# Kernel tuning notes

Measured on AMD Instinct MI355X. Metric: run time of the kernel, lower is better.

The kernel has to match this reference:

```python
import jax, jax.numpy as jnp
import numpy as np
from fractions import Fraction
from math import factorial

MUL = 64
IRREPS = [(MUL, 0, 1), (MUL, 1, -1), (MUL, 2, 1)]  # (mul, l, parity); same for in1/in2/out
N = 4096


def _f(n):
    return Fraction(factorial(round(n)), 1)


def _su2_cg(j1, m1, j2, m2, j3, m3):
    # Complex-basis SU(2) Clebsch-Gordan coefficient <j1 m1 j2 m2 | j3 m3> (Racah formula).
    if m3 != m1 + m2:
        return 0.0
    vmin = int(max(-j1 + j2 + m3, -j1 + m1, 0))
    vmax = int(min(j2 + j3 + m1, j3 - j1 + j2, j3 + m3))
    C = float((2 * j3 + 1) * Fraction(
        _f(j3 + j1 - j2) * _f(j3 - j1 + j2) * _f(j1 + j2 - j3) * _f(j3 + m3) * _f(j3 - m3),
        _f(j1 + j2 + j3 + 1) * _f(j1 - m1) * _f(j1 + m1) * _f(j2 - m2) * _f(j2 + m2))) ** 0.5
    S = Fraction(0)
    for v in range(vmin, vmax + 1):
        S += (-1) ** int(v + j2 + m2) * Fraction(
            _f(j2 + j3 + m1 - v) * _f(j1 - m1 + v),
            _f(v) * _f(j3 - j1 + j2 - v) * _f(j3 + m3 - v) * _f(v + j1 - j2 - m3))
    return C * float(S)


def _q(l):
    # Change of basis real -> complex spherical harmonics, with (-i)^l phase so CG is real.
    q = np.zeros((2 * l + 1, 2 * l + 1), dtype=complex)
    for m in range(-l, 0):
        q[l + m, l + abs(m)] = 1 / 2 ** 0.5
        q[l + m, l - abs(m)] = -1j / 2 ** 0.5
    q[l, l] = 1
    for m in range(1, l + 1):
        q[l + m, l + abs(m)] = (-1) ** m / 2 ** 0.5
        q[l + m, l - abs(m)] = 1j * (-1) ** m / 2 ** 0.5
    return (-1j) ** l * q


def _so3_cg(l1, l2, l3):
    # Real-basis SO(3) Clebsch-Gordan tensor, shape (2l1+1, 2l2+1, 2l3+1).
    C = np.zeros((2 * l1 + 1, 2 * l2 + 1, 2 * l3 + 1))
    for m1 in range(-l1, l1 + 1):
        for m2 in range(-l2, l2 + 1):
            for m3 in range(-l3, l3 + 1):
                C[l1 + m1, l2 + m2, l3 + m3] = _su2_cg(l1, m1, l2, m2, l3, m3)
    C = np.einsum('ij,kl,mn,ikm->jln', _q(l1), _q(l2), np.conj(_q(l3)), C)
    assert np.abs(C.imag).max() < 1e-6
    return np.ascontiguousarray(C.real.astype(np.float32))


def _offsets(irreps):
    offs, o = [], 0
    for mul, l, p in irreps:
        offs.append(o)
        o += mul * (2 * l + 1)
    return offs, o


OFF, DIM = _offsets(IRREPS)

# Enumerate fully-connected paths honoring parity and triangle selection rules.
PATHS = []
for io, (mo, lo, po) in enumerate(IRREPS):
    for i1, (m1, l1, p1) in enumerate(IRREPS):
        for i2, (m2, l2, p2) in enumerate(IRREPS):
            if p1 * p2 == po and abs(l1 - l2) <= lo <= l1 + l2:
                PATHS.append((i1, i2, io, _so3_cg(l1, l2, lo)))
N_PATHS = len(PATHS)  # 11 for this irrep layout


def setup_inputs() -> dict:
    key = jax.random.key(0)
    k1, k2, k3 = jax.random.split(key, 3)
    inputs1 = jax.random.normal(k1, (N, DIM), dtype=jnp.float32)
    inputs2 = jax.random.normal(k2, (N, DIM), dtype=jnp.float32)
    std = 1.0 / float(np.sqrt(MUL * MUL))  # per-path weight_std
    W = jax.random.normal(k3, (N_PATHS, MUL, MUL, MUL), dtype=jnp.float32) * std
    return {"inputs1": inputs1, "inputs2": inputs2, "W": W}


def _seg(x, i):
    mul, l, _ = IRREPS[i]
    d = 2 * l + 1
    return x[:, OFF[i]:OFF[i] + mul * d].reshape(x.shape[0], mul, d)


def reference(inputs1, inputs2, W):
    # out[z, w, k] = sum_{u,v,i,j} W_path[u,v,w] * CG[i,j,k] * x1[z,u,i] * x2[z,v,j]
    segs = [[] for _ in IRREPS]
    for p, (i1, i2, io, cg) in enumerate(PATHS):
        x1 = _seg(inputs1, i1)  # [z, u, i]
        x2 = _seg(inputs2, i2)  # [z, v, j]
        y = jnp.einsum('zui,zvj,ijk,uvw->zwk', x1, x2, jnp.asarray(cg), W[p], optimize=True)
        segs[io].append(y)
    out = jnp.concatenate(
        [sum(s).reshape(inputs1.shape[0], -1) for s in segs], axis=-1)
    # normalize=True: divide by sqrt(output dim), as in the source
    return out * (1.0 / float(np.sqrt(out.shape[-1])))
```

## Files before the change

kernel.cpp:

```cpp
#include <hip/hip_runtime.h>
#include <hip/hip_fp16.h>


typedef unsigned short u16;
typedef _Float16 f16;
typedef __attribute__((ext_vector_type(8))) _Float16 f16x8;
typedef __attribute__((ext_vector_type(4))) float f32x4;

#define NZ 4096
#define ROWE 832
#define ROW2 576

__device__ __forceinline__ u16 f2h(float x) {
    _Float16 v = (_Float16)x; u16 b; __builtin_memcpy(&b, &v, 2); return b;
}

constexpr u16 f2h_bits(float xf) {
    unsigned u = __builtin_bit_cast(unsigned, xf);
    unsigned sign = (u >> 16) & 0x8000u;
    int exp = (int)((u >> 23) & 0xffu) - 127 + 15;
    unsigned man = u & 0x7fffffu;
    if (exp >= 31) return (u16)(sign | 0x7c00u);
    if (exp <= 0) {
        if (exp < -10) return (u16)sign;
        man |= 0x800000u;
        int sh = 14 - exp;
        unsigned h = man >> sh;
        unsigned rem = man & ((1u << sh) - 1u);
        unsigned half = 1u << (sh - 1);
        if (rem > half || (rem == half && (h & 1u))) ++h;
        return (u16)(sign | h);
    }
    unsigned h = ((unsigned)exp << 10) | (man >> 13);
    unsigned rem = man & 0x1fffu;
    if (rem > 0x1000u || (rem == 0x1000u && (h & 1u))) ++h;
    return (u16)(sign | h);
}
__device__ __forceinline__ __half2 h2dup(unsigned bits16) {
    unsigned d = bits16 * 0x10001u;
    __half2 r; __builtin_memcpy(&r, &d, 4); return r;
}
__device__ __forceinline__ __half2 h2zero() {
    unsigned z = 0; __half2 r; __builtin_memcpy(&r, &z, 4); return r;
}

struct CGE { int i, j, k; float c; };
template<int P> struct CGT;
template<> struct CGT<0> { static constexpr int n=1; static constexpr CGE e[1]={{0,0,0,1.0f}}; };
template<> struct CGT<1> { static constexpr int n=3; static constexpr CGE e[3]={
    {0,0,0,0.5773502691896258f},{1,1,0,0.5773502691896258f},{2,2,0,0.5773502691896258f}}; };
template<> struct CGT<2> { static constexpr int n=5; static constexpr CGE e[5]={
    {0,0,0,0.4472135954999579f},{1,1,0,0.4472135954999579f},{2,2,0,0.4472135954999579f},
    {3,3,0,0.4472135954999579f},{4,4,0,0.4472135954999579f}}; };
template<> struct CGT<3> { static constexpr int n=3; static constexpr CGE e[3]={
    {0,0,0,1.0f},{0,1,1,1.0f},{0,2,2,1.0f}}; };
template<> struct CGT<4> { static constexpr int n=3; static constexpr CGE e[3]={
    {0,0,0,1.0f},{1,0,1,1.0f},{2,0,2,1.0f}}; };
template<> struct CGT<5> { static constexpr int n=11; static constexpr CGE e[11]={
    {0,2,0,-0.31622776601683794f},{1,1,0,0.5477225575051661f},{0,4,0,-0.5477225575051661f},{2,0,0,0.5477225575051661f},
    {0,1,1,0.5477225575051661f},{2,3,1,0.5477225575051661f},{1,2,1,0.6324555320336759f},
    {2,2,2,-0.31622776601683794f},{1,3,2,0.5477225575051661f},{0,0,2,0.5477225575051661f},{2,4,2,0.5477225575051661f}}; };
template<> struct CGT<6> { static constexpr int n=11; static constexpr CGE e[11]={
    {2,0,0,-0.31622776601683794f},{1,1,0,0.5477225575051661f},{4,0,0,-0.5477225575051661f},{0,2,0,0.5477225575051661f},
    {1,0,1,0.5477225575051661f},{3,2,1,0.5477225575051661f},{2,1,1,0.6324555320336759f},
    {2,2,2,-0.31622776601683794f},{3,1,2,0.5477225575051661f},{0,0,2,0.5477225575051661f},{4,2,2,0.5477225575051661f}}; };
template<> struct CGT<7> { static constexpr int n=5; static constexpr CGE e[5]={
    {0,0,0,1.0f},{0,1,1,1.0f},{0,2,2,1.0f},{0,3,3,1.0f},{0,4,4,1.0f}}; };
template<> struct CGT<8> { static constexpr int n=11; static constexpr CGE e[11]={
    {0,2,0,0.7071067811865476f},{2,0,0,0.7071067811865476f},
    {0,1,1,0.7071067811865476f},{1,0,1,0.7071067811865476f},
    {0,0,2,-0.4082482904638630f},{1,1,2,0.8164965809277260f},{2,2,2,-0.4082482904638630f},
    {1,2,3,0.7071067811865476f},{2,1,3,0.7071067811865476f},
    {0,0,4,-0.7071067811865476f},{2,2,4,0.7071067811865476f}}; };
template<> struct CGT<9> { static constexpr int n=5; static constexpr CGE e[5]={
    {0,0,0,1.0f},{1,0,1,1.0f},{2,0,2,1.0f},{3,0,3,1.0f},{4,0,4,1.0f}}; };
template<> struct CGT<10> { static constexpr int n=25; static constexpr CGE e[25]={
    {0,2,0,-0.5345224838248488f},{2,0,0,-0.5345224838248488f},{1,3,0,0.4629100498862757f},{3,1,0,0.4629100498862757f},
    {0,3,1,0.4629100498862757f},{3,0,1,0.4629100498862757f},{1,4,1,-0.4629100498862757f},{4,1,1,-0.4629100498862757f},
    {1,2,1,0.2672612419124244f},{2,1,1,0.2672612419124244f},
    {0,0,2,-0.5345224838248488f},{1,1,2,0.2672612419124244f},{2,2,2,0.5345224838248488f},{3,3,2,0.2672612419124244f},{4,4,2,-0.5345224838248488f},
    {0,1,3,0.4629100498862757f},{1,0,3,0.4629100498862757f},{3,4,3,0.4629100498862757f},{4,3,3,0.4629100498862757f},
    {2,3,3,0.2672612419124244f},{3,2,3,0.2672612419124244f},
    {1,1,4,-0.4629100498862757f},{3,3,4,0.4629100498862757f},{2,4,4,-0.5345224838248488f},{4,2,4,-0.5345224838248488f}}; };

template<int SEG>
__device__ __forceinline__ int soff(int m) {
    if constexpr (SEG == 0) return m;
    else if constexpr (SEG == 1) return 64 + 4*m;
    else return 320 + 8*m;
}
template<int SEG>
__device__ __forceinline__ int sb2(int j) {
    if constexpr (SEG == 0) return 0;
    else if constexpr (SEG == 1) return 64 + j*64;
    else return 256 + j*64;
}
template<int L>
__device__ __forceinline__ void load_a1bits(const u16* p, u16* o) {
    if constexpr (L == 0) {
        o[0] = p[0];
    } else if constexpr (L == 1) {
        uint2 r = *reinterpret_cast<const uint2*>(p);
        o[0] = (u16)(r.x & 0xffff); o[1] = (u16)(r.x >> 16); o[2] = (u16)(r.y & 0xffff);
    } else {
        uint4 r = *reinterpret_cast<const uint4*>(p);
        o[0] = (u16)(r.x & 0xffff); o[1] = (u16)(r.x >> 16);
        o[2] = (u16)(r.y & 0xffff); o[3] = (u16)(r.y >> 16);
        o[4] = (u16)(r.z & 0xffff);
    }
}

__device__ __forceinline__ void stage_chunk(const u16* __restrict__ Wtb, int g,
                                            u16* lbuf, int tid) {
    const u16* src = Wtb + ((size_t)g << 13);
    #pragma unroll
    for (int qq = 0; qq < 4; ++qq) {
        const int off = qq*2048 + tid*8;
        __builtin_amdgcn_global_load_lds(
            (const __attribute__((address_space(1))) void*)(const void*)(src + off),
            (__attribute__((address_space(3))) void*)(void*)(lbuf + off),
            16, 0, 0);
    }
}

template<int PID, int S1, int S2, int KO>
__device__ __forceinline__ void chunk_compute(const u16* __restrict__ lbuf,
                                              const u16 (&a1b)[2][2*S1+1],
                                              const __half2 (&b2h)[2][4][2*S2+1],
                                              f32x4 (&acc)[KO][4], int lane) {
    const int kb = lane >> 4, nl = lane & 15;
    #pragma unroll
    for (int uu = 0; uu < 2; ++uu) {
        __half2 a1h[2*S1+1];
        #pragma unroll
        for (int i = 0; i < 2*S1+1; ++i) a1h[i] = h2dup(a1b[uu][i]);
        __half2 pre[CGT<PID>::n];
        #pragma unroll
        for (int t = 0; t < CGT<PID>::n; ++t) {
            const u16 cb = f2h_bits(CGT<PID>::e[t].c);
            pre[t] = __hmul2(h2dup(cb), a1h[CGT<PID>::e[t].i]);
        }
        #pragma unroll
        for (int h = 0; h < 2; ++h) {
            f16x8 bf[4];
            #pragma unroll
            for (int nf = 0; nf < 4; ++nf) {
                const int w = nf*16 + nl;
                const int slot = w*16 + ((uu*8 + h*4 + kb) ^ (w & 15));
                bf[nf] = *reinterpret_cast<const f16x8*>(lbuf + slot*8);
            }
            #pragma unroll
            for (int ko = 0; ko < KO; ++ko) {
                union { __half2 h[4]; f16x8 v; } af;
                #pragma unroll
                for (int q = 0; q < 4; ++q) {
                    __half2 s = h2zero();
                    #pragma unroll
                    for (int t = 0; t < CGT<PID>::n; ++t)
                        if (CGT<PID>::e[t].k == ko)
                            s = __hfma2(pre[t], b2h[h][q][CGT<PID>::e[t].j], s);
                    af.h[q] = s;
                }
                #pragma unroll
                for (int nf = 0; nf < 4; ++nf)
                    acc[ko][nf] = __builtin_amdgcn_mfma_f32_16x16x32_f16(af.v, bf[nf], acc[ko][nf], 0, 0, 0);
            }
        }
    }
}

template<int PID, int S1, int S2, int KO>
__device__ __forceinline__ void run_path(const u16* __restrict__ x1r, const u16* __restrict__ x2r,
                                         const u16* __restrict__ Wtb, u16* lds,
                                         f32x4 (&acc)[KO][4], int lane, int tid,
                                         int cbase, int cpp, int& q, int nq, int GB) {
    constexpr int D1 = 2*S1 + 1, D2 = 2*S2 + 1;
    const int kb = lane >> 4;
    __half2 b2h[2][4][D2];
    #pragma unroll
    for (int h = 0; h < 2; ++h)
        #pragma unroll
        for (int j = 0; j < D2; ++j) {
            const u16* p = x2r + sb2<S2>(j) + h*32 + kb*8;
            uint4 r = *reinterpret_cast<const uint4*>(p);
            __builtin_memcpy(&b2h[h][0][j], &r.x, 4);
            __builtin_memcpy(&b2h[h][1][j], &r.y, 4);
            __builtin_memcpy(&b2h[h][2][j], &r.z, 4);
            __builtin_memcpy(&b2h[h][3][j], &r.w, 4);
        }

    const int ubase = cbase*2;
    u16 a1b[2][D1], a1nb[2][D1];
    #pragma unroll
    for (int uu = 0; uu < 2; ++uu)
        load_a1bits<S1>(x1r + soff<S1>(ubase + uu), a1b[uu]);

    for (int c = 0; c < cpp; ++c) {
        __syncthreads();
        const int cn = (c + 1 == cpp) ? 0 : c + 1;
        #pragma unroll
        for (int uu = 0; uu < 2; ++uu)
            load_a1bits<S1>(x1r + soff<S1>(ubase + cn*2 + uu), a1nb[uu]);
        if (q + 1 < nq) {
            const int qn = q + 1;
            const int g = GB + (qn/cpp)*32 + cbase + (qn % cpp);
            stage_chunk(Wtb, g, lds + ((qn & 1) << 13), tid);
        }
        chunk_compute<PID,S1,S2,KO>(lds + ((q & 1) << 13), a1b, b2h, acc, lane);
        #pragma unroll
        for (int uu = 0; uu < 2; ++uu)
            #pragma unroll
            for (int d = 0; d < D1; ++d) a1b[uu][d] = a1nb[uu][d];
        ++q;
    }
}

template<int IO, bool DIRECT>
__device__ __forceinline__ void run_unit(const u16* __restrict__ XB1, const u16* __restrict__ XB2,
                                         const u16* __restrict__ Wtb, float* __restrict__ dst,
                                         int zt, int cbase, int cpp, u16* lds) {
    constexpr int KO   = 2*IO + 1;
    constexpr int NP   = (IO == 0) ? 3 : 4;
    constexpr int GB   = (IO == 0) ? 0 : (IO == 1 ? 96 : 224);
    constexpr int OFFI = (IO == 0) ? 0 : (IO == 1 ? 64 : 256);
    constexpr int CO   = KO*64;
    const int tid = threadIdx.x;
    const int lane = tid & 63, wave = tid >> 6;
    const int zin = zt*64 + wave*16 + (lane & 15);
    const u16* x1r = XB1 + (size_t)zin*ROWE;
    const u16* x2r = XB2 + (size_t)zin*ROW2;
    f32x4 acc[KO][4];
    #pragma unroll
    for (int k = 0; k < KO; ++k)
        #pragma unroll
        for (int nf = 0; nf < 4; ++nf) acc[k][nf] = (f32x4){0.f, 0.f, 0.f, 0.f};

    int q = 0;
    const int nq = NP*cpp;
    stage_chunk(Wtb, GB + cbase, lds, tid);

    if constexpr (IO == 0) {
        run_path<0,0,0,KO>(x1r, x2r, Wtb, lds, acc, lane, tid, cbase, cpp, q, nq, GB);
        run_path<1,1,1,KO>(x1r, x2r, Wtb, lds, acc, lane, tid, cbase, cpp, q, nq, GB);
        run_path<2,2,2,KO>(x1r, x2r, Wtb, lds, acc, lane, tid, cbase, cpp, q, nq, GB);
    } else if constexpr (IO == 1) {
        run_path<3,0,1,KO>(x1r, x2r, Wtb, lds, acc, lane, tid, cbase, cpp, q, nq, GB);
        run_path<4,1,0,KO>(x1r, x2r, Wtb, lds, acc, lane, tid, cbase, cpp, q, nq, GB);
        run_path<5,1,2,KO>(x1r, x2r, Wtb, lds, acc, lane, tid, cbase, cpp, q, nq, GB);
        run_path<6,2,1,KO>(x1r, x2r, Wtb, lds, acc, lane, tid, cbase, cpp, q, nq, GB);
    } else {
        run_path<7,0,2,KO>(x1r, x2r, Wtb, lds, acc, lane, tid, cbase, cpp, q, nq, GB);
        run_path<8,1,1,KO>(x1r, x2r, Wtb, lds, acc, lane, tid, cbase, cpp, q, nq, GB);
        run_path<9,2,0,KO>(x1r, x2r, Wtb, lds, acc, lane, tid, cbase, cpp, q, nq, GB);
        run_path<10,2,2,KO>(x1r, x2r, Wtb, lds, acc, lane, tid, cbase, cpp, q, nq, GB);
    }

    float* lf = reinterpret_cast<float*>(lds);
    const int nl = lane & 15;
    const int hi = lane >> 4;
    #pragma unroll
    for (int round = 0; round < 4; ++round) {
        __syncthreads();
        if (wave == round) {
            const int zl = hi*4;
            #pragma unroll
            for (int k = 0; k < KO; ++k)
                #pragma unroll
                for (int nf = 0; nf < 4; ++nf) {
                    const int col = (nf*16 + nl)*KO + k;
                    #pragma unroll
                    for (int r = 0; r < 4; ++r)
                        lf[(zl + r)*CO + col] = acc[k][nf][r];
                }
        }
        __syncthreads();
        const int zbase = zt*64 + round*16;
        const int TOT4 = 4*CO;
        for (int i = tid; i < TOT4; i += 256) {
            const int zr = i / (CO/4), c4 = i % (CO/4);
            float4 v = *reinterpret_cast<const float4*>(&lf[zr*CO + c4*4]);
            if constexpr (DIRECT) {
                const float sc = 0.041666666666666664f;
                v.x *= sc; v.y *= sc; v.z *= sc; v.w *= sc;
            }
            *reinterpret_cast<float4*>(&dst[(size_t)(zbase + zr)*576 + OFFI + c4*4]) = v;
        }
    }
}

template<bool DIRECT>
__global__ __launch_bounds__(256) void tp_main(const u16* __restrict__ XB1, const u16* __restrict__ XB2,
                                               const u16* __restrict__ Wtb, float* __restrict__ dst) {
    __shared__ u16 smem[2*8192];
    const int bid = blockIdx.x;
    int io, uq, zt, cbase, cpp;
    if constexpr (DIRECT) {
        io = 2 - (bid >> 6); zt = bid & 63; uq = 0; cbase = 0; cpp = 32;
    } else {
        if (bid < 256)      { io = 2; uq = bid >> 6;         zt = bid & 63; cbase = uq*8; cpp = 8; }
        else if (bid < 448) { int b = bid - 256; io = 1; uq = b >> 6; zt = b & 63;
                              cbase = (uq == 0) ? 0 : (11 + 11*(uq - 1)); cpp = (uq == 2) ? 10 : 11; }
        else                { int b = bid - 448; io = 0; uq = 0; zt = b; cbase = 0; cpp = 32; }
    }
    float* dstP = DIRECT ? dst : dst + (size_t)uq*NZ*576;
    if (io == 0)      run_unit<0,DIRECT>(XB1, XB2, Wtb, dstP, zt, cbase, cpp, smem);
    else if (io == 1) run_unit<1,DIRECT>(XB1, XB2, Wtb, dstP, zt, cbase, cpp, smem);
    else              run_unit<2,DIRECT>(XB1, XB2, Wtb, dstP, zt, cbase, cpp, smem);
}

__global__ __launch_bounds__(256) void reduce_k(const float* __restrict__ P, float* __restrict__ out) {
    const int i = blockIdx.x*256 + threadIdx.x;
    const int col0 = (i*4) % 576;
    const int cnt = (col0 < 64) ? 1 : (col0 < 256 ? 3 : 4);
    float4 s = reinterpret_cast<const float4*>(P)[i];
    for (int u = 1; u < cnt; ++u) {
        float4 t = reinterpret_cast<const float4*>(P + (size_t)u*NZ*576)[i];
        s.x += t.x; s.y += t.y; s.z += t.z; s.w += t.w;
    }
    const float sc = 0.041666666666666664f;
    float4 o; o.x = s.x*sc; o.y = s.y*sc; o.z = s.z*sc; o.w = s.w*sc;
    reinterpret_cast<float4*>(out)[i] = o;
}

__global__ void prep_x(const float* __restrict__ x1, const float* __restrict__ x2,
                       u16* __restrict__ XB1, u16* __restrict__ XB2) {
    int g = blockIdx.x * 256 + threadIdx.x;
    const int P1 = NZ * 192;
    const int P2 = NZ * 144;
    if (g < P1) {
        const int zz = g / 192, s = g - zz*192, seg = s >> 6, m = s & 63;
        const float* sp = x1 + (size_t)zz*576;
        u16* dp = XB1 + (size_t)zz*ROWE;
        if (seg == 0) {
            dp[m] = f2h(sp[m]);
        } else if (seg == 1) {
            u16 t0 = f2h(sp[64 + m*3 + 0]);
            u16 t1 = f2h(sp[64 + m*3 + 1]);
            u16 t2 = f2h(sp[64 + m*3 + 2]);
            uint2 pk; pk.x = (unsigned)t0 | ((unsigned)t1 << 16); pk.y = (unsigned)t2;
            *reinterpret_cast<uint2*>(dp + 64 + m*4) = pk;
        } else {
            u16 t[5];
            #pragma unroll
            for (int c = 0; c < 5; ++c) t[c] = f2h(sp[256 + m*5 + c]);
            uint4 pk;
            pk.x = (unsigned)t[0] | ((unsigned)t[1] << 16);
            pk.y = (unsigned)t[2] | ((unsigned)t[3] << 16);
            pk.z = (unsigned)t[4];
            pk.w = 0u;
            *reinterpret_cast<uint4*>(dp + 320 + m*8) = pk;
        }
    } else if (g < P1 + P2) {
        const int gg = g - P1;
        const int zz = gg / 144, c4 = gg - zz*144;
        const int col = c4*4;
        const float* sp = x2 + (size_t)zz*576;
        u16 t[4];
        #pragma unroll
        for (int qd = 0; qd < 4; ++qd) {
            const int cc = col + qd;
            int si;
            if (cc < 64)       si = cc;
            else if (cc < 256) { const int j = (cc - 64) >> 6, v = (cc - 64) & 63;  si = 64  + v*3 + j; }
            else               { const int j = (cc - 256) >> 6, v = (cc - 256) & 63; si = 256 + v*5 + j; }
            t[qd] = f2h(sp[si]);
        }
        uint2 pk;
        pk.x = (unsigned)t[0] | ((unsigned)t[1] << 16);
        pk.y = (unsigned)t[2] | ((unsigned)t[3] << 16);
        *reinterpret_cast<uint2*>(XB2 + (size_t)zz*ROW2 + col) = pk;
    }
}

__global__ void prep_w(const float* __restrict__ W, u16* __restrict__ Wtb) {
    __shared__ float ld[4096];
    const int b = blockIdx.x;
    const int p = b >> 6, u = b & 63;
    const int tid = threadIdx.x;
    const float* src = W + ((size_t)(p*64 + u) << 12);
    #pragma unroll
    for (int i = 0; i < 16; ++i) ld[tid + i*256] = src[tid + i*256];
    __syncthreads();
    const int g  = p*32 + (u >> 1);
    const int mb = (u & 1)*8;
    #pragma unroll
    for (int r = 0; r < 2; ++r) {
        const int j = r*256 + tid;
        const int w = j & 63, ms = j >> 6;
        const int m = mb + ms;
        const int h = ms >> 2, kb = ms & 3;
        const int vb = h*32 + kb*8;
        u16 tmp[8];
        #pragma unroll
        for (int e = 0; e < 8; ++e) tmp[e] = f2h(ld[(vb + e)*64 + w]);
        const int unit = w*16 + (m ^ (w & 15));
        uint4 pk;
        pk.x = (unsigned)tmp[0] | ((unsigned)tmp[1] << 16);
        pk.y = (unsigned)tmp[2] | ((unsigned)tmp[3] << 16);
        pk.z = (unsigned)tmp[4] | ((unsigned)tmp[5] << 16);
        pk.w = (unsigned)tmp[6] | ((unsigned)tmp[7] << 16);
        *reinterpret_cast<uint4*>(Wtb + (size_t)g*8192 + (size_t)unit*8) = pk;
    }
}

extern "C" void kernel_launch(void* const* d_in, const int* in_sizes, int n_in,
                              void* d_out, int out_size, void* d_ws, size_t ws_size,
                              hipStream_t stream) {
    const float* x1 = (const float*)d_in[0];
    const float* x2 = (const float*)d_in[1];
    const float* W  = (const float*)d_in[2];
    float* out = (float*)d_out;

    u16* XB1 = (u16*)d_ws;
    u16* XB2 = XB1 + (size_t)NZ*ROWE;
    u16* Wtb = XB2 + (size_t)NZ*ROW2;
    const size_t baseu = (size_t)NZ*ROWE + (size_t)NZ*ROW2 + (size_t)11*32*8192;
    if (ws_size < baseu*2) return;
    float* Pbuf = (float*)(XB1 + baseu);
    const size_t avail = ws_size - baseu*2;
    const size_t psz = (size_t)NZ*576*4;
    const bool balanced = (avail >= 4*psz);

    hipLaunchKernelGGL(prep_x, dim3((NZ*(192+144))/256), dim3(256), 0, stream, x1, x2, XB1, XB2);
    hipLaunchKernelGGL(prep_w, dim3(11*64), dim3(256), 0, stream, W, Wtb);

    if (balanced) {
        hipLaunchKernelGGL(tp_main<false>, dim3(512), dim3(256), 0, stream, XB1, XB2, Wtb, Pbuf);
        hipLaunchKernelGGL(reduce_k, dim3(NZ*576/4/256), dim3(256), 0, stream, Pbuf, out);
    } else {
        hipLaunchKernelGGL(tp_main<true>, dim3(192), dim3(256), 0, stream, XB1, XB2, Wtb, out);
    }
}
```

Measured before the change: 112.7 us.

## Split output m-components across blocks and write split-K partials directly

The main kernel's work is repartitioned so each block handles only a subrange of output m-components (KOB..KOE). This doubles the grid from 512 to 1024 blocks and shrinks the accumulator register footprint per block. The l=0 output is now split into two u-halves, so reduce_k sums two partials for those columns. Non-bounce units store accumulators straight to global memory instead of staging through LDS. This removes syncs but gives strided scalar stores, and each split block repeats the x-operand and CG preprocessing.

```diff
diff --git a/kernel.cpp b/kernel.cpp
--- a/kernel.cpp
+++ b/kernel.cpp
@@ -123,11 +123,11 @@
     }
 }
 
-template<int PID, int S1, int S2, int KO>
+template<int PID, int S1, int S2, int KOB, int KOE>
 __device__ __forceinline__ void chunk_compute(const u16* __restrict__ lbuf,
                                               const u16 (&a1b)[2][2*S1+1],
                                               const __half2 (&b2h)[2][4][2*S2+1],
-                                              f32x4 (&acc)[KO][4], int lane) {
+                                              f32x4 (&acc)[KOE-KOB][4], int lane) {
     const int kb = lane >> 4, nl = lane & 15;
     #pragma unroll
     for (int uu = 0; uu < 2; ++uu) {
@@ -150,29 +150,29 @@
                 bf[nf] = *reinterpret_cast<const f16x8*>(lbuf + slot*8);
             }
             #pragma unroll
-            for (int ko = 0; ko < KO; ++ko) {
+            for (int koi = 0; koi < KOE-KOB; ++koi) {
                 union { __half2 h[4]; f16x8 v; } af;
                 #pragma unroll
                 for (int q = 0; q < 4; ++q) {
                     __half2 s = h2zero();
                     #pragma unroll
                     for (int t = 0; t < CGT<PID>::n; ++t)
-                        if (CGT<PID>::e[t].k == ko)
+                        if (CGT<PID>::e[t].k == KOB + koi)
                             s = __hfma2(pre[t], b2h[h][q][CGT<PID>::e[t].j], s);
                     af.h[q] = s;
                 }
                 #pragma unroll
                 for (int nf = 0; nf < 4; ++nf)
-                    acc[ko][nf] = __builtin_amdgcn_mfma_f32_16x16x32_f16(af.v, bf[nf], acc[ko][nf], 0, 0, 0);
+                    acc[koi][nf] = __builtin_amdgcn_mfma_f32_16x16x32_f16(af.v, bf[nf], acc[koi][nf], 0, 0, 0);
             }
         }
     }
 }
 
-template<int PID, int S1, int S2, int KO>
+template<int PID, int S1, int S2, int KOB, int KOE>
 __device__ __forceinline__ void run_path(const u16* __restrict__ x1r, const u16* __restrict__ x2r,
                                          const u16* __restrict__ Wtb, u16* lds,
-                                         f32x4 (&acc)[KO][4], int lane, int tid,
+                                         f32x4 (&acc)[KOE-KOB][4], int lane, int tid,
                                          int cbase, int cpp, int& q, int nq, int GB) {
     constexpr int D1 = 2*S1 + 1, D2 = 2*S2 + 1;
     const int kb = lane >> 4;
@@ -206,7 +206,7 @@
             const int g = GB + (qn/cpp)*32 + cbase + (qn % cpp);
             stage_chunk(Wtb, g, lds + ((qn & 1) << 13), tid);
         }
-        chunk_compute<PID,S1,S2,KO>(lds + ((q & 1) << 13), a1b, b2h, acc, lane);
+        chunk_compute<PID,S1,S2,KOB,KOE>(lds + ((q & 1) << 13), a1b, b2h, acc, lane);
         #pragma unroll
         for (int uu = 0; uu < 2; ++uu)
             #pragma unroll
@@ -215,7 +215,7 @@
     }
 }
 
-template<int IO, bool DIRECT>
+template<int IO, int KOB, int KOE, bool BOUNCE, bool DIRECT>
 __device__ __forceinline__ void run_unit(const u16* __restrict__ XB1, const u16* __restrict__ XB2,
                                          const u16* __restrict__ Wtb, float* __restrict__ dst,
                                          int zt, int cbase, int cpp, u16* lds) {
@@ -223,15 +223,15 @@
     constexpr int NP   = (IO == 0) ? 3 : 4;
     constexpr int GB   = (IO == 0) ? 0 : (IO == 1 ? 96 : 224);
     constexpr int OFFI = (IO == 0) ? 0 : (IO == 1 ? 64 : 256);
-    constexpr int CO   = KO*64;
+    constexpr int NK   = KOE - KOB;
     const int tid = threadIdx.x;
     const int lane = tid & 63, wave = tid >> 6;
     const int zin = zt*64 + wave*16 + (lane & 15);
     const u16* x1r = XB1 + (size_t)zin*ROWE;
     const u16* x2r = XB2 + (size_t)zin*ROW2;
-    f32x4 acc[KO][4];
-    #pragma unroll
-    for (int k = 0; k < KO; ++k)
+    f32x4 acc[NK][4];
+    #pragma unroll
+    for (int k = 0; k < NK; ++k)
         #pragma unroll
         for (int nf = 0; nf < 4; ++nf) acc[k][nf] = (f32x4){0.f, 0.f, 0.f, 0.f};
 
@@ -240,78 +240,104 @@
     stage_chunk(Wtb, GB + cbase, lds, tid);
 
     if constexpr (IO == 0) {
-        run_path<0,0,0,KO>(x1r, x2r, Wtb, lds, acc, lane, tid, cbase, cpp, q, nq, GB);
-        run_path<1,1,1,KO>(x1r, x2r, Wtb, lds, acc, lane, tid, cbase, cpp, q, nq, GB);
-        run_path<2,2,2,KO>(x1r, x2r, Wtb, lds, acc, lane, tid, cbase, cpp, q, nq, GB);
+        run_path<0,0,0,KOB,KOE>(x1r, x2r, Wtb, lds, acc, lane, tid, cbase, cpp, q, nq, GB);
+        run_path<1,1,1,KOB,KOE>(x1r, x2r, Wtb, lds, acc, lane, tid, cbase, cpp, q, nq, GB);
+        run_path<2,2,2,KOB,KOE>(x1r, x2r, Wtb, lds, acc, lane, tid, cbase, cpp, q, nq, GB);
     } else if constexpr (IO == 1) {
-        run_path<3,0,1,KO>(x1r, x2r, Wtb, lds, acc, lane, tid, cbase, cpp, q, nq, GB);
-        run_path<4,1,0,KO>(x1r, x2r, Wtb, lds, acc, lane, tid, cbase, cpp, q, nq, GB);
-        run_path<5,1,2,KO>(x1r, x2r, Wtb, lds, acc, lane, tid, cbase, cpp, q, nq, GB);
-        run_path<6,2,1,KO>(x1r, x2r, Wtb, lds, acc, lane, tid, cbase, cpp, q, nq, GB);
+        run_path<3,0,1,KOB,KOE>(x1r, x2r, Wtb, lds, acc, lane, tid, cbase, cpp, q, nq, GB);
+        run_path<4,1,0,KOB,KOE>(x1r, x2r, Wtb, lds, acc, lane, tid, cbase, cpp, q, nq, GB);
+        run_path<5,1,2,KOB,KOE>(x1r, x2r, Wtb, lds, acc, lane, tid, cbase, cpp, q, nq, GB);
+        run_path<6,2,1,KOB,KOE>(x1r, x2r, Wtb, lds, acc, lane, tid, cbase, cpp, q, nq, GB);
     } else {
-        run_path<7,0,2,KO>(x1r, x2r, Wtb, lds, acc, lane, tid, cbase, cpp, q, nq, GB);
-        run_path<8,1,1,KO>(x1r, x2r, Wtb, lds, acc, lane, tid, cbase, cpp, q, nq, GB);
-        run_path<9,2,0,KO>(x1r, x2r, Wtb, lds, acc, lane, tid, cbase, cpp, q, nq, GB);
-        run_path<10,2,2,KO>(x1r, x2r, Wtb, lds, acc, lane, tid, cbase, cpp, q, nq, GB);
-    }
-
-    float* lf = reinterpret_cast<float*>(lds);
+        run_path<7,0,2,KOB,KOE>(x1r, x2r, Wtb, lds, acc, lane, tid, cbase, cpp, q, nq, GB);
+        run_path<8,1,1,KOB,KOE>(x1r, x2r, Wtb, lds, acc, lane, tid, cbase, cpp, q, nq, GB);
+        run_path<9,2,0,KOB,KOE>(x1r, x2r, Wtb, lds, acc, lane, tid, cbase, cpp, q, nq, GB);
+        run_path<10,2,2,KOB,KOE>(x1r, x2r, Wtb, lds, acc, lane, tid, cbase, cpp, q, nq, GB);
+    }
+
     const int nl = lane & 15;
-    const int hi = lane >> 4;
-    #pragma unroll
-    for (int round = 0; round < 4; ++round) {
-        __syncthreads();
-        if (wave == round) {
-            const int zl = hi*4;
+    if constexpr (BOUNCE) {
+        constexpr int CO = KO*64;
+        float* lf = reinterpret_cast<float*>(lds);
+        const int hi = lane >> 4;
+        #pragma unroll
+        for (int round = 0; round < 4; ++round) {
+            __syncthreads();
+            if (wave == round) {
+                const int zl = hi*4;
+                #pragma unroll
+                for (int k = 0; k < NK; ++k)
+                    #pragma unroll
+                    for (int nf = 0; nf < 4; ++nf) {
+                        const int col = (nf*16 + nl)*KO + k;
+                        #pragma unroll
+                        for (int r = 0; r < 4; ++r)
+                            lf[(zl + r)*CO + col] = acc[k][nf][r];
+                    }
+            }
+            __syncthreads();
+            const int zbase = zt*64 + round*16;
+            const int TOT4 = 4*CO;
+            for (int i = tid; i < TOT4; i += 256) {
+                const int zr = i / (CO/4), c4 = i % (CO/4);
+                float4 v = *reinterpret_cast<const float4*>(&lf[zr*CO + c4*4]);
+                if constexpr (DIRECT) {
+                    const float sc = 0.041666666666666664f;
+                    v.x *= sc; v.y *= sc; v.z *= sc; v.w *= sc;
+                }
+                *reinterpret_cast<float4*>(&dst[(size_t)(zbase + zr)*576 + OFFI + c4*4]) = v;
+            }
+        }
+    } else {
+        const int zoutb = zt*64 + wave*16 + (lane >> 4)*4;
+        #pragma unroll
+        for (int k = 0; k < NK; ++k)
             #pragma unroll
-            for (int k = 0; k < KO; ++k)
+            for (int nf = 0; nf < 4; ++nf) {
+                const int wcol = nf*16 + nl;
                 #pragma unroll
-                for (int nf = 0; nf < 4; ++nf) {
-                    const int col = (nf*16 + nl)*KO + k;
-                    #pragma unroll
-                    for (int r = 0; r < 4; ++r)
-                        lf[(zl + r)*CO + col] = acc[k][nf][r];
-                }
-        }
-        __syncthreads();
-        const int zbase = zt*64 + round*16;
-        const int TOT4 = 4*CO;
-        for (int i = tid; i < TOT4; i += 256) {
-            const int zr = i / (CO/4), c4 = i % (CO/4);
-            float4 v = *reinterpret_cast<const float4*>(&lf[zr*CO + c4*4]);
-            if constexpr (DIRECT) {
-                const float sc = 0.041666666666666664f;
-                v.x *= sc; v.y *= sc; v.z *= sc; v.w *= sc;
+                for (int r = 0; r < 4; ++r)
+                    dst[(size_t)(zoutb + r)*576 + OFFI + wcol*KO + KOB + k] = acc[k][nf][r];
             }
-            *reinterpret_cast<float4*>(&dst[(size_t)(zbase + zr)*576 + OFFI + c4*4]) = v;
-        }
-    }
-}
-
-template<bool DIRECT>
-__global__ __launch_bounds__(256) void tp_main(const u16* __restrict__ XB1, const u16* __restrict__ XB2,
-                                               const u16* __restrict__ Wtb, float* __restrict__ dst) {
+    }
+}
+
+__global__ __launch_bounds__(256) void tp_main_split(const u16* __restrict__ XB1, const u16* __restrict__ XB2,
+                                                     const u16* __restrict__ Wtb, float* __restrict__ Pbuf) {
     __shared__ u16 smem[2*8192];
     const int bid = blockIdx.x;
-    int io, uq, zt, cbase, cpp;
-    if constexpr (DIRECT) {
-        io = 2 - (bid >> 6); zt = bid & 63; uq = 0; cbase = 0; cpp = 32;
+    if (bid < 256) {
+        const int zt = bid & 63, uq = bid >> 6;
+        run_unit<2,0,3,false,false>(XB1, XB2, Wtb, Pbuf + (size_t)uq*NZ*576, zt, uq*8, 8, smem);
+    } else if (bid < 448) {
+        const int b = bid - 256, zt = b & 63, uq = b >> 6;
+        run_unit<1,0,2,false,false>(XB1, XB2, Wtb, Pbuf + (size_t)uq*NZ*576, zt, uq*11, (uq == 2) ? 10 : 11, smem);
+    } else if (bid < 704) {
+        const int b = bid - 448, zt = b & 63, uq = b >> 6;
+        run_unit<2,3,5,false,false>(XB1, XB2, Wtb, Pbuf + (size_t)uq*NZ*576, zt, uq*8, 8, smem);
+    } else if (bid < 896) {
+        const int b = bid - 704, zt = b & 63, uq = b >> 6;
+        run_unit<1,2,3,false,false>(XB1, XB2, Wtb, Pbuf + (size_t)uq*NZ*576, zt, uq*11, (uq == 2) ? 10 : 11, smem);
     } else {
-        if (bid < 256)      { io = 2; uq = bid >> 6;         zt = bid & 63; cbase = uq*8; cpp = 8; }
-        else if (bid < 448) { int b = bid - 256; io = 1; uq = b >> 6; zt = b & 63;
-                              cbase = (uq == 0) ? 0 : (11 + 11*(uq - 1)); cpp = (uq == 2) ? 10 : 11; }
-        else                { int b = bid - 448; io = 0; uq = 0; zt = b; cbase = 0; cpp = 32; }
-    }
-    float* dstP = DIRECT ? dst : dst + (size_t)uq*NZ*576;
-    if (io == 0)      run_unit<0,DIRECT>(XB1, XB2, Wtb, dstP, zt, cbase, cpp, smem);
-    else if (io == 1) run_unit<1,DIRECT>(XB1, XB2, Wtb, dstP, zt, cbase, cpp, smem);
-    else              run_unit<2,DIRECT>(XB1, XB2, Wtb, dstP, zt, cbase, cpp, smem);
+        const int b = bid - 896, zt = b & 63, uq = b >> 6;
+        run_unit<0,0,1,true,false>(XB1, XB2, Wtb, Pbuf + (size_t)uq*NZ*576, zt, uq*16, 16, smem);
+    }
+}
+
+__global__ __launch_bounds__(256) void tp_main_direct(const u16* __restrict__ XB1, const u16* __restrict__ XB2,
+                                                      const u16* __restrict__ Wtb, float* __restrict__ out) {
+    __shared__ u16 smem[2*8192];
+    const int bid = blockIdx.x;
+    const int io = 2 - (bid >> 6), zt = bid & 63;
+    if (io == 0)      run_unit<0,0,1,true,true>(XB1, XB2, Wtb, out, zt, 0, 32, smem);
+    else if (io == 1) run_unit<1,0,3,true,true>(XB1, XB2, Wtb, out, zt, 0, 32, smem);
+    else              run_unit<2,0,5,true,true>(XB1, XB2, Wtb, out, zt, 0, 32, smem);
 }
 
 __global__ __launch_bounds__(256) void reduce_k(const float* __restrict__ P, float* __restrict__ out) {
     const int i = blockIdx.x*256 + threadIdx.x;
     const int col0 = (i*4) % 576;
-    const int cnt = (col0 < 64) ? 1 : (col0 < 256 ? 3 : 4);
+    const int cnt = (col0 < 64) ? 2 : (col0 < 256 ? 3 : 4);
     float4 s = reinterpret_cast<const float4*>(P)[i];
     for (int u = 1; u < cnt; ++u) {
         float4 t = reinterpret_cast<const float4*>(P + (size_t)u*NZ*576)[i];
@@ -425,9 +451,9 @@
     hipLaunchKernelGGL(prep_w, dim3(11*64), dim3(256), 0, stream, W, Wtb);
 
     if (balanced) {
-        hipLaunchKernelGGL(tp_main<false>, dim3(512), dim3(256), 0, stream, XB1, XB2, Wtb, Pbuf);
+        hipLaunchKernelGGL(tp_main_split, dim3(1024), dim3(256), 0, stream, XB1, XB2, Wtb, Pbuf);
         hipLaunchKernelGGL(reduce_k, dim3(NZ*576/4/256), dim3(256), 0, stream, Pbuf, out);
     } else {
-        hipLaunchKernelGGL(tp_main<true>, dim3(192), dim3(256), 0, stream, XB1, XB2, Wtb, out);
-    }
-}
+        hipLaunchKernelGGL(tp_main_direct, dim3(192), dim3(256), 0, stream, XB1, XB2, Wtb, out);
+    }
+}
```

New measurement: 131.6 us. +16.8%, slower.
